# Optimization experiments

Hardware: AMD Instinct MI355X
Metric: run time of the kernel (lower is better)

Reference implementation:

```python
import jax, jax.numpy as jnp
import numpy as np

B, S, H, O, L = 32, 4096, 256, 256, 2


def setup_inputs() -> dict:
    key = jax.random.key(0)
    ks = jax.random.split(key, 12)
    s = 0.05  # weight init scale
    return {
        "input": jax.random.normal(ks[0], (B, S, H), dtype=jnp.float32),
        "hidden_state": jnp.zeros((B, L, H), dtype=jnp.float32),
        # gate weights, stacked over layers: [L, H_out, H_in] (torch Linear convention)
        "Wxz": jax.random.normal(ks[1], (L, H, H), dtype=jnp.float32) * s,
        "Whz": jax.random.normal(ks[2], (L, H, H), dtype=jnp.float32) * s,
        "bz": jax.random.normal(ks[3], (L, H), dtype=jnp.float32) * s,
        "Wxr": jax.random.normal(ks[4], (L, H, H), dtype=jnp.float32) * s,
        "Whr": jax.random.normal(ks[5], (L, H, H), dtype=jnp.float32) * s,
        "br": jax.random.normal(ks[6], (L, H), dtype=jnp.float32) * s,
        "Wxg": jax.random.normal(ks[7], (L, H, H), dtype=jnp.float32) * s,
        "Whg": jax.random.normal(ks[8], (L, H, H), dtype=jnp.float32) * s,
        "bg": jax.random.normal(ks[9], (L, H), dtype=jnp.float32) * s,
        "Why": jax.random.normal(ks[10], (O, H), dtype=jnp.float32) * s,
        "by": jax.random.normal(ks[11], (O,), dtype=jnp.float32) * s,
    }


def _gru_forward(x, h0, Wxz, Whz, bz, Wxr, Whr, br, Wxg, Whg, bg, Why, by):
    # x: [B,S,I], h0: [B,L,H]
    n_layers = Wxz.shape[0]
    xs = jnp.swapaxes(x, 0, 1)          # [S,B,I]
    h_init = jnp.swapaxes(h0, 0, 1)     # [L,B,H]

    def step(h, x_t):                    # h: [L,B,H], x_t: [B,I]
        inp = x_t
        new_h = []
        for l in range(n_layers):
            hl = h[l]
            z = jax.nn.sigmoid(inp @ Wxz[l].T + hl @ Whz[l].T + bz[l])
            r = jax.nn.sigmoid(inp @ Wxr[l].T + hl @ Whr[l].T + br[l])
            g = jnp.tanh(inp @ Wxg[l].T + (hl * r) @ Whg[l].T + bg[l])
            hn = z * hl + (1.0 - z) * g
            new_h.append(hn)
            inp = hn  # dropout p=0 -> identity
        y_t = inp @ Why.T + by           # [B,O]
        return jnp.stack(new_h), y_t

    h_final, ys = jax.lax.scan(step, h_init, xs)
    layer_output = jnp.swapaxes(ys, 0, 1)        # [B,S,O]
    hidden_state = jnp.swapaxes(h_final, 0, 1)   # [B,L,H]
    return layer_output, hidden_state


def reference(input, hidden_state, Wxz, Whz, bz, Wxr, Whr, br, Wxg, Whg, bg, Why, by):
    return _gru_forward(input, hidden_state, Wxz, Whz, bz, Wxr, Whr, br, Wxg, Whg, bg, Why, by)
```

## Files before the change

### kernel.cpp

```cpp
#include <hip/hip_runtime.h>


typedef __attribute__((ext_vector_type(8))) short short8;
typedef __attribute__((ext_vector_type(4))) float f32x4;

#define TC      256
#define NCHUNK  16
#define SSZ     4096
#define LW      (256*256)

#define SIGSC  (-1.44269504089f)
#define TANHSC ( 2.88539008178f)

__device__ __forceinline__ float bf2f(unsigned short u) {
    union { unsigned int i; float f; } v; v.i = ((unsigned int)u) << 16; return v.f;
}
__device__ __forceinline__ unsigned short f2bf(float f) {
    union { float f; unsigned int i; } v; v.f = f;
    v.i += 0x7fff + ((v.i >> 16) & 1);
    return (unsigned short)(v.i >> 16);
}
__device__ __forceinline__ unsigned int pkbf(float lo, float hi) {
    union { float f; unsigned int i; } a, b; a.f = lo; b.f = hi;
    return __builtin_amdgcn_perm(b.i + 0x8000u, a.i + 0x8000u, 0x07060302);
}
__device__ __forceinline__ short8 cvt8s(const float* p, float s) {
    float4 a = *(const float4*)p;
    float4 b = *(const float4*)(p + 4);
    short8 r;
    r[0] = (short)f2bf(a.x * s); r[1] = (short)f2bf(a.y * s);
    r[2] = (short)f2bf(a.z * s); r[3] = (short)f2bf(a.w * s);
    r[4] = (short)f2bf(b.x * s); r[5] = (short)f2bf(b.y * s);
    r[6] = (short)f2bf(b.z * s); r[7] = (short)f2bf(b.w * s);
    return r;
}
__device__ __forceinline__ void wg_barrier() {
    asm volatile("s_waitcnt lgkmcnt(0)" ::: "memory");
    __builtin_amdgcn_s_barrier();
}

__global__ __launch_bounds__(256, 2) void gemm3(
    const float* __restrict__ x,
    const unsigned short* __restrict__ Hc0, const unsigned short* __restrict__ Hc1,
    const float* __restrict__ Wxz, const float* __restrict__ Wxr, const float* __restrict__ Wxg,
    const float* __restrict__ bz,  const float* __restrict__ br,  const float* __restrict__ bg,
    const float* __restrict__ Why, const float* __restrict__ by,
    unsigned short* __restrict__ XS0, unsigned short* __restrict__ XS1,
    float* __restrict__ out, int c)
{
    __shared__ unsigned short Alds[64 * 256];
    __shared__ unsigned short Wlds[64 * 256];

    const int jt = blockIdx.y;
    const void* Aptr; int a_mode, c0abs = 0, o_mode, jtl;
    const float *w0, *w1, *w2, *b0, *b1, *b2; void* Optr;
    if (jt < 12) {
        if (c > 15) return;
        Aptr = x; a_mode = 0; c0abs = c * TC;
        w0 = Wxz; w1 = Wxr; w2 = Wxg; b0 = bz; b1 = br; b2 = bg;
        Optr = XS0; o_mode = 0; jtl = jt;
    } else if (jt < 24) {
        if (c < 1 || c > 16) return;
        Aptr = Hc0; a_mode = 1;
        w0 = Wxz + LW; w1 = Wxr + LW; w2 = Wxg + LW;
        b0 = bz + 256; b1 = br + 256; b2 = bg + 256;
        Optr = XS1; o_mode = 0; jtl = jt - 12;
    } else {
        if (c < 2) return;
        Aptr = Hc1; a_mode = 1; c0abs = (c - 2) * TC;
        w0 = Why; w1 = Why; w2 = Why; b0 = by; b1 = by; b2 = by;
        Optr = out; o_mode = 1; jtl = jt - 24;
    }

    const int tid = threadIdx.x;
    const int mt = blockIdx.x;

    for (int idx = tid; idx < 4096; idx += 256) {
        int row = idx >> 6;
        int kq  = (idx & 63) << 2;
        int sw  = row * 256 + (((((kq >> 3) ^ (row & 7)) << 3)) | (kq & 7));
        if (a_mode == 0) {
            int i = mt * 64 + row; int tc = i >> 5, b = i & 31;
            const float* p = (const float*)Aptr + ((size_t)b * SSZ + (size_t)(c0abs + tc)) * 256 + kq;
            float4 v = *(const float4*)p;
            ushort4 u; u.x = f2bf(v.x); u.y = f2bf(v.y); u.z = f2bf(v.z); u.w = f2bf(v.w);
            *(ushort4*)&Alds[sw] = u;
        } else {
            const unsigned short* p = (const unsigned short*)Aptr + (size_t)(mt * 64 + row) * 256 + kq;
            *(ushort4*)&Alds[sw] = *(const ushort4*)p;
        }
    }
    for (int idx = tid; idx < 4096; idx += 256) {
        int row = idx >> 6;
        int kq  = (idx & 63) << 2;
        int j   = jtl * 64 + row;
        const float* wp = (j < 256) ? w0 : ((j < 512) ? w1 : w2);
        const float* p  = wp + (size_t)(j & 255) * 256 + kq;
        float4 v = *(const float4*)p;
        ushort4 u; u.x = f2bf(v.x); u.y = f2bf(v.y); u.z = f2bf(v.z); u.w = f2bf(v.w);
        int sw = row * 256 + (((((kq >> 3) ^ (row & 7)) << 3)) | (kq & 7));
        *(ushort4*)&Wlds[sw] = u;
    }
    __syncthreads();

    const int lane = tid & 63, wv = tid >> 6;
    const int cl = lane & 15, qr = lane >> 4;
    f32x4 acc[4];
    #pragma unroll
    for (int nt = 0; nt < 4; ++nt) acc[nt] = (f32x4){0.f, 0.f, 0.f, 0.f};

    #pragma unroll
    for (int kt = 0; kt < 8; ++kt) {
        int kb = kt * 4 + qr;
        short8 af = *(const short8*)&Alds[(wv * 16 + cl) * 256 + ((kb ^ (cl & 7)) << 3)];
        #pragma unroll
        for (int nt = 0; nt < 4; ++nt) {
            short8 bf = *(const short8*)&Wlds[(nt * 16 + cl) * 256 + ((kb ^ (cl & 7)) << 3)];
            acc[nt] = __builtin_amdgcn_mfma_f32_16x16x32_bf16(af, bf, acc[nt], 0, 0, 0);
        }
    }

    #pragma unroll
    for (int nt = 0; nt < 4; ++nt) {
        int j = jtl * 64 + nt * 16 + cl;
        const float* bp = (j < 256) ? b0 : ((j < 512) ? b1 : b2);
        float bias = bp[j & 255];
        #pragma unroll
        for (int r = 0; r < 4; ++r) {
            float v = acc[nt][r] + bias;
            int m = mt * 64 + wv * 16 + qr * 4 + r;
            if (o_mode == 0) {
                int t = m >> 5, b = m & 31;
                int wgs = b >> 4, scl = b & 15;
                int gate = j >> 8, cc = j & 255;
                int swv = cc >> 5, snt = (cc >> 4) & 1, sqr = (cc >> 2) & 3, sr = cc & 3;
                int stid = swv * 64 + sqr * 16 + scl;
                size_t off = (((size_t)((t * 2 + wgs) * 3 + gate)) << 12)
                           + (size_t)stid * 8 + (snt * 4 + sr);
                float gs = (gate < 2) ? SIGSC : TANHSC;
                ((unsigned short*)Optr)[off] = f2bf(v * gs);
            } else {
                int tc = m >> 5, b = m & 31;
                ((float*)Optr)[(size_t)b * (SSZ * 256) + (size_t)(c0abs + tc) * 256 + j] = v;
            }
        }
    }
}

__global__ __launch_bounds__(512, 2) void scan_dual(
    const unsigned short* __restrict__ XS0, const unsigned short* __restrict__ XS1,
    unsigned short* __restrict__ Hc0, unsigned short* __restrict__ Hc1,
    float* __restrict__ hstate,
    const float* __restrict__ hidden_in,
    const float* __restrict__ Whz0, const float* __restrict__ Whr0,
    const float* __restrict__ Whg0,
    int c, float* __restrict__ dout_tail)
{
    __shared__ unsigned short hA[4096];
    __shared__ unsigned short A2[4096];
    __shared__ unsigned short Wg[65536];

    const int layer = blockIdx.x >> 1;
    const int wg    = blockIdx.x & 1;
    const int chunk = (layer == 0) ? c : c - 1;
    if (chunk < 0 || chunk > 15) return;

    const unsigned short* XS = (layer == 0) ? XS0 : XS1;
    unsigned short* Hout     = (layer == 0) ? Hc0 : Hc1;
    const float* Whz = Whz0 + (size_t)layer * LW;
    const float* Whr = Whr0 + (size_t)layer * LW;
    const float* Whg = Whg0 + (size_t)layer * LW;
    const int first_chunk = (chunk == 0), last_chunk = (chunk == NCHUNK - 1);

    const int tid  = threadIdx.x;
    const int lane = tid & 63, wv = tid >> 6;
    const int cl   = lane & 15, qr = lane >> 4;
    const int swl  = cl & 7;
    const int b    = wg * 16 + cl;

    for (int idx = tid; idx < 16384; idx += 512) {
        int n  = idx >> 6;
        int kq = (idx & 63) << 2;
        float4 v = *(const float4*)(Whg + (size_t)n * 256 + kq);
        ushort4 u;
        u.x = f2bf(v.x * TANHSC); u.y = f2bf(v.y * TANHSC);
        u.z = f2bf(v.z * TANHSC); u.w = f2bf(v.w * TANHSC);
        int sw = n * 256 + (((((kq >> 3) ^ (n & 7)) << 3)) | (kq & 7));
        *(ushort4*)&Wg[sw] = u;
    }

    short8 wzf[2][8], wrf[2][8];
    #pragma unroll
    for (int nt = 0; nt < 2; ++nt) {
        int n = wv * 32 + nt * 16 + cl;
        #pragma unroll
        for (int kt = 0; kt < 8; ++kt) {
            int k0 = kt * 32 + qr * 8;
            wzf[nt][kt] = cvt8s(Whz + (size_t)n * 256 + k0, SIGSC);
            wrf[nt][kt] = cvt8s(Whr + (size_t)n * 256 + k0, SIGSC);
        }
    }

    int wro[2];
    #pragma unroll
    for (int nt = 0; nt < 2; ++nt) {
        int nb = wv * 32 + nt * 16 + qr * 4;
        wro[nt] = cl * 256 + ((((nb >> 3) ^ swl) << 3) | (nb & 4));
    }

    float hreg[2][4];
    #pragma unroll
    for (int nt = 0; nt < 2; ++nt) {
        int nb = wv * 32 + nt * 16 + qr * 4;
        float4 h4;
        if (first_chunk) h4 = *(const float4*)(hidden_in + (size_t)b * 512 + layer * 256 + nb);
        else             h4 = *(const float4*)(hstate + layer * 8192 + b * 256 + nb);
        hreg[nt][0] = h4.x; hreg[nt][1] = h4.y; hreg[nt][2] = h4.z; hreg[nt][3] = h4.w;
        uint2 p; p.x = pkbf(h4.x, h4.y); p.y = pkbf(h4.z, h4.w);
        *(uint2*)&hA[wro[nt]] = p;
    }

    const unsigned short* xp = XS + (size_t)wg * 12288 + (size_t)tid * 8;
    short8 xz = *(const short8*)(xp);
    short8 xr = *(const short8*)(xp + 4096);
    short8 xg = *(const short8*)(xp + 8192);

    wg_barrier();

    uint2 hpk[2];
    const size_t holane = (size_t)(wg * 16 + cl) * 256 + (size_t)wv * 32 + (size_t)qr * 4;

    #pragma unroll 1
    for (int t = 0; t < TC; ++t) {
        if (t) {
            unsigned short* hp = Hout + (size_t)(t - 1) * 8192 + holane;
            *(uint2*)hp        = hpk[0];
            *(uint2*)(hp + 16) = hpk[1];
        }

        const unsigned short* xq = xp + (size_t)((t + 1 < TC) ? t + 1 : t) * 24576;
        short8 nz = *(const short8*)(xq);
        short8 nr = *(const short8*)(xq + 4096);
        short8 ng = *(const short8*)(xq + 8192);

        f32x4 az[2], ar[2];
        #pragma unroll
        for (int nt = 0; nt < 2; ++nt) {
            #pragma unroll
            for (int r = 0; r < 4; ++r) {
                az[nt][r] = bf2f((unsigned short)xz[nt * 4 + r]);
                ar[nt][r] = bf2f((unsigned short)xr[nt * 4 + r]);
            }
        }
        #pragma unroll
        for (int kt = 0; kt < 8; ++kt) {
            int kb = kt * 4 + qr;
            short8 bf = *(const short8*)&hA[cl * 256 + ((kb ^ swl) << 3)];
            az[0] = __builtin_amdgcn_mfma_f32_16x16x32_bf16(wzf[0][kt], bf, az[0], 0, 0, 0);
            ar[0] = __builtin_amdgcn_mfma_f32_16x16x32_bf16(wrf[0][kt], bf, ar[0], 0, 0, 0);
            az[1] = __builtin_amdgcn_mfma_f32_16x16x32_bf16(wzf[1][kt], bf, az[1], 0, 0, 0);
            ar[1] = __builtin_amdgcn_mfma_f32_16x16x32_bf16(wrf[1][kt], bf, ar[1], 0, 0, 0);
        }

        float zs[2][4];
        #pragma unroll
        for (int nt = 0; nt < 2; ++nt) {
            float a2v[4];
            #pragma unroll
            for (int r = 0; r < 4; ++r) {
                zs[nt][r] = __builtin_amdgcn_rcpf(1.0f + __builtin_amdgcn_exp2f(az[nt][r]));
                float rr  = __builtin_amdgcn_rcpf(1.0f + __builtin_amdgcn_exp2f(ar[nt][r]));
                a2v[r] = rr * hreg[nt][r];
            }
            uint2 p; p.x = pkbf(a2v[0], a2v[1]); p.y = pkbf(a2v[2], a2v[3]);
            *(uint2*)&A2[wro[nt]] = p;
        }
        wg_barrier();

        f32x4 ag[2];
        #pragma unroll
        for (int nt = 0; nt < 2; ++nt) {
            #pragma unroll
            for (int r = 0; r < 4; ++r)
                ag[nt][r] = bf2f((unsigned short)xg[nt * 4 + r]);
        }
        #pragma unroll
        for (int kt = 0; kt < 8; ++kt) {
            int kb = kt * 4 + qr;
            int ko = (kb ^ swl) << 3;
            short8 bf  = *(const short8*)&A2[cl * 256 + ko];
            short8 af0 = *(const short8*)&Wg[(wv * 32 + cl) * 256 + ko];
            short8 af1 = *(const short8*)&Wg[(wv * 32 + 16 + cl) * 256 + ko];
            ag[0] = __builtin_amdgcn_mfma_f32_16x16x32_bf16(af0, bf, ag[0], 0, 0, 0);
            ag[1] = __builtin_amdgcn_mfma_f32_16x16x32_bf16(af1, bf, ag[1], 0, 0, 0);
        }
        #pragma unroll
        for (int nt = 0; nt < 2; ++nt) {
            float hn4[4];
            #pragma unroll
            for (int r = 0; r < 4; ++r) {
                float g = 1.0f - 2.0f * __builtin_amdgcn_rcpf(
                              1.0f + __builtin_amdgcn_exp2f(ag[nt][r]));
                float hn = g + zs[nt][r] * (hreg[nt][r] - g);
                hreg[nt][r] = hn;
                hn4[r] = hn;
            }
            uint2 p; p.x = pkbf(hn4[0], hn4[1]); p.y = pkbf(hn4[2], hn4[3]);
            hpk[nt] = p;
            *(uint2*)&hA[wro[nt]] = p;
        }
        wg_barrier();

        xz = nz; xr = nr; xg = ng;
    }

    {
        unsigned short* hp = Hout + (size_t)(TC - 1) * 8192 + holane;
        *(uint2*)hp        = hpk[0];
        *(uint2*)(hp + 16) = hpk[1];
    }
    #pragma unroll
    for (int nt = 0; nt < 2; ++nt) {
        int nb = wv * 32 + nt * 16 + qr * 4;
        float4 h4; h4.x = hreg[nt][0]; h4.y = hreg[nt][1]; h4.z = hreg[nt][2]; h4.w = hreg[nt][3];
        *(float4*)(hstate + layer * 8192 + b * 256 + nb) = h4;
        if (last_chunk)
            *(float4*)(dout_tail + (size_t)b * 512 + layer * 256 + nb) = h4;
    }
}

extern "C" void kernel_launch(void* const* d_in, const int* in_sizes, int n_in,
                              void* d_out, int out_size, void* d_ws, size_t ws_size,
                              hipStream_t stream) {
    const float* x   = (const float*)d_in[0];
    const float* h0  = (const float*)d_in[1];
    const float* Wxz = (const float*)d_in[2];
    const float* Whz = (const float*)d_in[3];
    const float* bz  = (const float*)d_in[4];
    const float* Wxr = (const float*)d_in[5];
    const float* Whr = (const float*)d_in[6];
    const float* br  = (const float*)d_in[7];
    const float* Wxg = (const float*)d_in[8];
    const float* Whg = (const float*)d_in[9];
    const float* bg  = (const float*)d_in[10];
    const float* Why = (const float*)d_in[11];
    const float* by  = (const float*)d_in[12];
    float* out = (float*)d_out;

    char* ws = (char*)d_ws;
    unsigned short* bufA = (unsigned short*)(ws);
    unsigned short* bufB = (unsigned short*)(ws + 12582912);
    unsigned short* Hc0  = (unsigned short*)(ws + 25165824);
    unsigned short* Hc1  = (unsigned short*)(ws + 29360128);
    float*          hst  = (float*)(ws + 33554432);
    float* dout_tail = out + (size_t)32 * 4096 * 256;

    for (int i = 0; i <= 17; ++i) {
        gemm3<<<dim3(128, 28), 256, 0, stream>>>(x, Hc0, Hc1,
                                                 Wxz, Wxr, Wxg, bz, br, bg,
                                                 Why, by, bufA, bufB, out, i);
        if (i <= 16)
            scan_dual<<<4, 512, 0, stream>>>(bufA, bufB, Hc0, Hc1, hst, h0,
                                             Whz, Whr, Whg, i, dout_tail);
    }
}
```

Measured before the change: 9.550 ms.

## Fuse scan and projection GEMMs into one pipelined kernel with double buffers

```diff
diff --git a/kernel.cpp b/kernel.cpp
--- a/kernel.cpp
+++ b/kernel.cpp
@@ -4,10 +4,12 @@
 typedef __attribute__((ext_vector_type(8))) short short8;
 typedef __attribute__((ext_vector_type(4))) float f32x4;
 
-#define TC      256
-#define NCHUNK  16
+#define TC      128
+#define NCHUNK  32
 #define SSZ     4096
 #define LW      (256*256)
+#define XSPAR   3145728
+#define HPAR    1048576
 
 #define SIGSC  (-1.44269504089f)
 #define TANHSC ( 2.88539008178f)
@@ -39,58 +41,243 @@
     __builtin_amdgcn_s_barrier();
 }
 
-__global__ __launch_bounds__(256, 2) void gemm3(
-    const float* __restrict__ x,
-    const unsigned short* __restrict__ Hc0, const unsigned short* __restrict__ Hc1,
-    const float* __restrict__ Wxz, const float* __restrict__ Wxr, const float* __restrict__ Wxg,
-    const float* __restrict__ bz,  const float* __restrict__ br,  const float* __restrict__ bg,
+struct ScanS {
+    unsigned short hA[4096];
+    unsigned short A2[4096];
+    unsigned short WgL[65536];
+};
+struct GemmS {
+    unsigned short Alds[128 * 256];
+    unsigned short Wlds[64 * 256];
+};
+
+__global__ __launch_bounds__(512, 2) void fused(
+    const float* __restrict__ x, const float* __restrict__ h0,
+    const float* __restrict__ Wxz, const float* __restrict__ Whz, const float* __restrict__ bz,
+    const float* __restrict__ Wxr, const float* __restrict__ Whr, const float* __restrict__ br,
+    const float* __restrict__ Wxg, const float* __restrict__ Whg, const float* __restrict__ bg,
     const float* __restrict__ Why, const float* __restrict__ by,
-    unsigned short* __restrict__ XS0, unsigned short* __restrict__ XS1,
-    float* __restrict__ out, int c)
+    unsigned short* __restrict__ XS0b, unsigned short* __restrict__ XS1b,
+    unsigned short* __restrict__ Hc0b, unsigned short* __restrict__ Hc1b,
+    float* __restrict__ hst, float* __restrict__ out,
+    float* __restrict__ dout_tail, int i)
 {
-    __shared__ unsigned short Alds[64 * 256];
-    __shared__ unsigned short Wlds[64 * 256];
-
-    const int jt = blockIdx.y;
-    const void* Aptr; int a_mode, c0abs = 0, o_mode, jtl;
+    __shared__ union { ScanS s; GemmS g; } sm;
+
+    const int bid = blockIdx.x;
+    const int tid = threadIdx.x;
+
+    if (bid < 4) {
+        const int layer = bid >> 1;
+        const int wg    = bid & 1;
+        const int chunk = (layer == 0) ? i : i - 2;
+        if ((unsigned)chunk > 31u) return;
+
+        const unsigned short* XS = ((layer == 0) ? XS0b : XS1b) + (size_t)(chunk & 1) * XSPAR;
+        unsigned short* Hout     = ((layer == 0) ? Hc0b : Hc1b) + (size_t)(chunk & 1) * HPAR;
+        const float* Whz_l = Whz + (size_t)layer * LW;
+        const float* Whr_l = Whr + (size_t)layer * LW;
+        const float* Whg_l = Whg + (size_t)layer * LW;
+        const int first_chunk = (chunk == 0), last_chunk = (chunk == NCHUNK - 1);
+
+        unsigned short* hA  = sm.s.hA;
+        unsigned short* A2  = sm.s.A2;
+        unsigned short* WgL = sm.s.WgL;
+
+        const int lane = tid & 63, wv = tid >> 6;
+        const int cl   = lane & 15, qr = lane >> 4;
+        const int swl  = cl & 7;
+        const int b    = wg * 16 + cl;
+
+        for (int idx = tid; idx < 8192; idx += 512) {
+            int lane_s = idx & 63, kt = (idx >> 6) & 7, ntv = (idx >> 9) & 1, wvv = idx >> 10;
+            int n  = wvv * 32 + ntv * 16 + (lane_s & 15);
+            int k0 = kt * 32 + (lane_s >> 4) * 8;
+            short8 f = cvt8s(Whg_l + (size_t)n * 256 + k0, TANHSC);
+            *(short8*)&WgL[(size_t)idx * 8] = f;
+        }
+
+        short8 wzf[2][8], wrf[2][8];
+        #pragma unroll
+        for (int nt = 0; nt < 2; ++nt) {
+            int n = wv * 32 + nt * 16 + cl;
+            #pragma unroll
+            for (int kt = 0; kt < 8; ++kt) {
+                int k0 = kt * 32 + qr * 8;
+                wzf[nt][kt] = cvt8s(Whz_l + (size_t)n * 256 + k0, SIGSC);
+                wrf[nt][kt] = cvt8s(Whr_l + (size_t)n * 256 + k0, SIGSC);
+            }
+        }
+
+        int wro[2];
+        #pragma unroll
+        for (int nt = 0; nt < 2; ++nt) {
+            int nb = wv * 32 + nt * 16 + qr * 4;
+            wro[nt] = cl * 256 + ((((nb >> 3) ^ swl) << 3) | (nb & 4));
+        }
+
+        float hreg[2][4];
+        #pragma unroll
+        for (int nt = 0; nt < 2; ++nt) {
+            int nb = wv * 32 + nt * 16 + qr * 4;
+            float4 h4;
+            if (first_chunk) h4 = *(const float4*)(h0 + (size_t)b * 512 + layer * 256 + nb);
+            else             h4 = *(const float4*)(hst + layer * 8192 + b * 256 + nb);
+            hreg[nt][0] = h4.x; hreg[nt][1] = h4.y; hreg[nt][2] = h4.z; hreg[nt][3] = h4.w;
+            uint2 p; p.x = pkbf(h4.x, h4.y); p.y = pkbf(h4.z, h4.w);
+            *(uint2*)&hA[wro[nt]] = p;
+        }
+
+        const unsigned short* xp = XS + (size_t)wg * 12288 + (size_t)tid * 8;
+        short8 xz = *(const short8*)(xp);
+        short8 xr = *(const short8*)(xp + 4096);
+        short8 xg = *(const short8*)(xp + 8192);
+
+        wg_barrier();
+
+        uint2 hpk[2];
+        const size_t holane = (size_t)(wg * 16 + cl) * 256 + (size_t)wv * 32 + (size_t)qr * 4;
+
+        #pragma unroll 1
+        for (int t = 0; t < TC; ++t) {
+            if (t) {
+                unsigned short* hp = Hout + (size_t)(t - 1) * 8192 + holane;
+                *(uint2*)hp        = hpk[0];
+                *(uint2*)(hp + 16) = hpk[1];
+            }
+
+            const unsigned short* xq = xp + (size_t)((t + 1 < TC) ? t + 1 : t) * 24576;
+            short8 nz = *(const short8*)(xq);
+            short8 nr = *(const short8*)(xq + 4096);
+            short8 ng = *(const short8*)(xq + 8192);
+
+            f32x4 az[2], ar[2];
+            #pragma unroll
+            for (int nt = 0; nt < 2; ++nt) {
+                #pragma unroll
+                for (int r = 0; r < 4; ++r) {
+                    az[nt][r] = bf2f((unsigned short)xz[nt * 4 + r]);
+                    ar[nt][r] = bf2f((unsigned short)xr[nt * 4 + r]);
+                }
+            }
+            #pragma unroll
+            for (int kt = 0; kt < 8; ++kt) {
+                int kb = kt * 4 + qr;
+                short8 bf = *(const short8*)&hA[cl * 256 + ((kb ^ swl) << 3)];
+                az[0] = __builtin_amdgcn_mfma_f32_16x16x32_bf16(wzf[0][kt], bf, az[0], 0, 0, 0);
+                ar[0] = __builtin_amdgcn_mfma_f32_16x16x32_bf16(wrf[0][kt], bf, ar[0], 0, 0, 0);
+                az[1] = __builtin_amdgcn_mfma_f32_16x16x32_bf16(wzf[1][kt], bf, az[1], 0, 0, 0);
+                ar[1] = __builtin_amdgcn_mfma_f32_16x16x32_bf16(wrf[1][kt], bf, ar[1], 0, 0, 0);
+            }
+
+            float zs[2][4];
+            #pragma unroll
+            for (int nt = 0; nt < 2; ++nt) {
+                float a2v[4];
+                #pragma unroll
+                for (int r = 0; r < 4; ++r) {
+                    zs[nt][r] = __builtin_amdgcn_rcpf(1.0f + __builtin_amdgcn_exp2f(az[nt][r]));
+                    float rr  = __builtin_amdgcn_rcpf(1.0f + __builtin_amdgcn_exp2f(ar[nt][r]));
+                    a2v[r] = rr * hreg[nt][r];
+                }
+                uint2 p; p.x = pkbf(a2v[0], a2v[1]); p.y = pkbf(a2v[2], a2v[3]);
+                *(uint2*)&A2[wro[nt]] = p;
+            }
+            wg_barrier();
+
+            f32x4 ag[2];
+            #pragma unroll
+            for (int nt = 0; nt < 2; ++nt) {
+                #pragma unroll
+                for (int r = 0; r < 4; ++r)
+                    ag[nt][r] = bf2f((unsigned short)xg[nt * 4 + r]);
+            }
+            #pragma unroll
+            for (int kt = 0; kt < 8; ++kt) {
+                int kb = kt * 4 + qr;
+                int ko = (wv * 16 + kt) * 512 + lane * 8;
+                short8 bf  = *(const short8*)&A2[cl * 256 + ((kb ^ swl) << 3)];
+                short8 af0 = *(const short8*)&WgL[ko];
+                short8 af1 = *(const short8*)&WgL[ko + 4096];
+                ag[0] = __builtin_amdgcn_mfma_f32_16x16x32_bf16(af0, bf, ag[0], 0, 0, 0);
+                ag[1] = __builtin_amdgcn_mfma_f32_16x16x32_bf16(af1, bf, ag[1], 0, 0, 0);
+            }
+            #pragma unroll
+            for (int nt = 0; nt < 2; ++nt) {
+                float hn4[4];
+                #pragma unroll
+                for (int r = 0; r < 4; ++r) {
+                    float g = 1.0f - 2.0f * __builtin_amdgcn_rcpf(
+                                  1.0f + __builtin_amdgcn_exp2f(ag[nt][r]));
+                    float hn = g + zs[nt][r] * (hreg[nt][r] - g);
+                    hreg[nt][r] = hn;
+                    hn4[r] = hn;
+                }
+                uint2 p; p.x = pkbf(hn4[0], hn4[1]); p.y = pkbf(hn4[2], hn4[3]);
+                hpk[nt] = p;
+                *(uint2*)&hA[wro[nt]] = p;
+            }
+            wg_barrier();
+
+            xz = nz; xr = nr; xg = ng;
+        }
+
+        {
+            unsigned short* hp = Hout + (size_t)(TC - 1) * 8192 + holane;
+            *(uint2*)hp        = hpk[0];
+            *(uint2*)(hp + 16) = hpk[1];
+        }
+        #pragma unroll
+        for (int nt = 0; nt < 2; ++nt) {
+            int nb = wv * 32 + nt * 16 + qr * 4;
+            float4 h4; h4.x = hreg[nt][0]; h4.y = hreg[nt][1]; h4.z = hreg[nt][2]; h4.w = hreg[nt][3];
+            *(float4*)(hst + layer * 8192 + b * 256 + nb) = h4;
+            if (last_chunk)
+                *(float4*)(dout_tail + (size_t)b * 512 + layer * 256 + nb) = h4;
+        }
+        return;
+    }
+
+    const int gb = bid - 4;
+    const void* Aptr; int a_mode, c0abs = 0, o_mode, jtl, mtb;
     const float *w0, *w1, *w2, *b0, *b1, *b2; void* Optr;
-    if (jt < 12) {
-        if (c > 15) return;
-        Aptr = x; a_mode = 0; c0abs = c * TC;
+    if (gb < 384) {
+        int c = i + 1; if ((unsigned)c > 31u) return;
+        a_mode = 0; Aptr = x; c0abs = c * TC;
         w0 = Wxz; w1 = Wxr; w2 = Wxg; b0 = bz; b1 = br; b2 = bg;
-        Optr = XS0; o_mode = 0; jtl = jt;
-    } else if (jt < 24) {
-        if (c < 1 || c > 16) return;
-        Aptr = Hc0; a_mode = 1;
+        Optr = XS0b + (size_t)(c & 1) * XSPAR; o_mode = 0; jtl = gb >> 5; mtb = gb & 31;
+    } else if (gb < 768) {
+        int c = i - 1; if ((unsigned)c > 31u) return;
+        a_mode = 1; Aptr = Hc0b + (size_t)(c & 1) * HPAR;
         w0 = Wxz + LW; w1 = Wxr + LW; w2 = Wxg + LW;
         b0 = bz + 256; b1 = br + 256; b2 = bg + 256;
-        Optr = XS1; o_mode = 0; jtl = jt - 12;
+        Optr = XS1b + (size_t)(c & 1) * XSPAR; o_mode = 0; jtl = (gb - 384) >> 5; mtb = (gb - 384) & 31;
     } else {
-        if (c < 2) return;
-        Aptr = Hc1; a_mode = 1; c0abs = (c - 2) * TC;
+        int c = i - 3; if ((unsigned)c > 31u) return;
+        a_mode = 1; Aptr = Hc1b + (size_t)(c & 1) * HPAR; c0abs = c * TC;
         w0 = Why; w1 = Why; w2 = Why; b0 = by; b1 = by; b2 = by;
-        Optr = out; o_mode = 1; jtl = jt - 24;
-    }
-
-    const int tid = threadIdx.x;
-    const int mt = blockIdx.x;
-
-    for (int idx = tid; idx < 4096; idx += 256) {
+        Optr = out; o_mode = 1; jtl = (gb - 768) >> 5; mtb = (gb - 768) & 31;
+    }
+
+    unsigned short* Alds = sm.g.Alds;
+    unsigned short* Wlds = sm.g.Wlds;
+
+    for (int idx = tid; idx < 8192; idx += 512) {
         int row = idx >> 6;
         int kq  = (idx & 63) << 2;
         int sw  = row * 256 + (((((kq >> 3) ^ (row & 7)) << 3)) | (kq & 7));
         if (a_mode == 0) {
-            int i = mt * 64 + row; int tc = i >> 5, b = i & 31;
-            const float* p = (const float*)Aptr + ((size_t)b * SSZ + (size_t)(c0abs + tc)) * 256 + kq;
+            int i0 = mtb * 128 + row; int tc = i0 >> 5, bb = i0 & 31;
+            const float* p = (const float*)Aptr + ((size_t)bb * SSZ + (size_t)(c0abs + tc)) * 256 + kq;
             float4 v = *(const float4*)p;
             ushort4 u; u.x = f2bf(v.x); u.y = f2bf(v.y); u.z = f2bf(v.z); u.w = f2bf(v.w);
             *(ushort4*)&Alds[sw] = u;
         } else {
-            const unsigned short* p = (const unsigned short*)Aptr + (size_t)(mt * 64 + row) * 256 + kq;
+            const unsigned short* p = (const unsigned short*)Aptr + (size_t)(mtb * 128 + row) * 256 + kq;
             *(ushort4*)&Alds[sw] = *(const ushort4*)p;
         }
     }
-    for (int idx = tid; idx < 4096; idx += 256) {
+    for (int idx = tid; idx < 4096; idx += 512) {
         int row = idx >> 6;
         int kq  = (idx & 63) << 2;
         int j   = jtl * 64 + row;
@@ -105,6 +292,7 @@
 
     const int lane = tid & 63, wv = tid >> 6;
     const int cl = lane & 15, qr = lane >> 4;
+    const int sub = wv >> 2, wq = wv & 3;
     f32x4 acc[4];
     #pragma unroll
     for (int nt = 0; nt < 4; ++nt) acc[nt] = (f32x4){0.f, 0.f, 0.f, 0.f};
@@ -112,7 +300,7 @@
     #pragma unroll
     for (int kt = 0; kt < 8; ++kt) {
         int kb = kt * 4 + qr;
-        short8 af = *(const short8*)&Alds[(wv * 16 + cl) * 256 + ((kb ^ (cl & 7)) << 3)];
+        short8 af = *(const short8*)&Alds[(sub * 64 + wq * 16 + cl) * 256 + ((kb ^ (cl & 7)) << 3)];
         #pragma unroll
         for (int nt = 0; nt < 4; ++nt) {
             short8 bf = *(const short8*)&Wlds[(nt * 16 + cl) * 256 + ((kb ^ (cl & 7)) << 3)];
@@ -128,10 +316,10 @@
         #pragma unroll
         for (int r = 0; r < 4; ++r) {
             float v = acc[nt][r] + bias;
-            int m = mt * 64 + wv * 16 + qr * 4 + r;
+            int m = mtb * 128 + sub * 64 + wq * 16 + qr * 4 + r;
             if (o_mode == 0) {
-                int t = m >> 5, b = m & 31;
-                int wgs = b >> 4, scl = b & 15;
+                int t = m >> 5, bb = m & 31;
+                int wgs = bb >> 4, scl = bb & 15;
                 int gate = j >> 8, cc = j & 255;
                 int swv = cc >> 5, snt = (cc >> 4) & 1, sqr = (cc >> 2) & 3, sr = cc & 3;
                 int stid = swv * 64 + sqr * 16 + scl;
@@ -140,192 +328,10 @@
                 float gs = (gate < 2) ? SIGSC : TANHSC;
                 ((unsigned short*)Optr)[off] = f2bf(v * gs);
             } else {
-                int tc = m >> 5, b = m & 31;
-                ((float*)Optr)[(size_t)b * (SSZ * 256) + (size_t)(c0abs + tc) * 256 + j] = v;
-            }
-        }
-    }
-}
-
-__global__ __launch_bounds__(512, 2) void scan_dual(
-    const unsigned short* __restrict__ XS0, const unsigned short* __restrict__ XS1,
-    unsigned short* __restrict__ Hc0, unsigned short* __restrict__ Hc1,
-    float* __restrict__ hstate,
-    const float* __restrict__ hidden_in,
-    const float* __restrict__ Whz0, const float* __restrict__ Whr0,
-    const float* __restrict__ Whg0,
-    int c, float* __restrict__ dout_tail)
-{
-    __shared__ unsigned short hA[4096];
-    __shared__ unsigned short A2[4096];
-    __shared__ unsigned short Wg[65536];
-
-    const int layer = blockIdx.x >> 1;
-    const int wg    = blockIdx.x & 1;
-    const int chunk = (layer == 0) ? c : c - 1;
-    if (chunk < 0 || chunk > 15) return;
-
-    const unsigned short* XS = (layer == 0) ? XS0 : XS1;
-    unsigned short* Hout     = (layer == 0) ? Hc0 : Hc1;
-    const float* Whz = Whz0 + (size_t)layer * LW;
-    const float* Whr = Whr0 + (size_t)layer * LW;
-    const float* Whg = Whg0 + (size_t)layer * LW;
-    const int first_chunk = (chunk == 0), last_chunk = (chunk == NCHUNK - 1);
-
-    const int tid  = threadIdx.x;
-    const int lane = tid & 63, wv = tid >> 6;
-    const int cl   = lane & 15, qr = lane >> 4;
-    const int swl  = cl & 7;
-    const int b    = wg * 16 + cl;
-
-    for (int idx = tid; idx < 16384; idx += 512) {
-        int n  = idx >> 6;
-        int kq = (idx & 63) << 2;
-        float4 v = *(const float4*)(Whg + (size_t)n * 256 + kq);
-        ushort4 u;
-        u.x = f2bf(v.x * TANHSC); u.y = f2bf(v.y * TANHSC);
-        u.z = f2bf(v.z * TANHSC); u.w = f2bf(v.w * TANHSC);
-        int sw = n * 256 + (((((kq >> 3) ^ (n & 7)) << 3)) | (kq & 7));
-        *(ushort4*)&Wg[sw] = u;
-    }
-
-    short8 wzf[2][8], wrf[2][8];
-    #pragma unroll
-    for (int nt = 0; nt < 2; ++nt) {
-        int n = wv * 32 + nt * 16 + cl;
-        #pragma unroll
-        for (int kt = 0; kt < 8; ++kt) {
-            int k0 = kt * 32 + qr * 8;
-            wzf[nt][kt] = cvt8s(Whz + (size_t)n * 256 + k0, SIGSC);
-            wrf[nt][kt] = cvt8s(Whr + (size_t)n * 256 + k0, SIGSC);
-        }
-    }
-
-    int wro[2];
-    #pragma unroll
-    for (int nt = 0; nt < 2; ++nt) {
-        int nb = wv * 32 + nt * 16 + qr * 4;
-        wro[nt] = cl * 256 + ((((nb >> 3) ^ swl) << 3) | (nb & 4));
-    }
-
-    float hreg[2][4];
-    #pragma unroll
-    for (int nt = 0; nt < 2; ++nt) {
-        int nb = wv * 32 + nt * 16 + qr * 4;
-        float4 h4;
-        if (first_chunk) h4 = *(const float4*)(hidden_in + (size_t)b * 512 + layer * 256 + nb);
-        else             h4 = *(const float4*)(hstate + layer * 8192 + b * 256 + nb);
-        hreg[nt][0] = h4.x; hreg[nt][1] = h4.y; hreg[nt][2] = h4.z; hreg[nt][3] = h4.w;
-        uint2 p; p.x = pkbf(h4.x, h4.y); p.y = pkbf(h4.z, h4.w);
-        *(uint2*)&hA[wro[nt]] = p;
-    }
-
-    const unsigned short* xp = XS + (size_t)wg * 12288 + (size_t)tid * 8;
-    short8 xz = *(const short8*)(xp);
-    short8 xr = *(const short8*)(xp + 4096);
-    short8 xg = *(const short8*)(xp + 8192);
-
-    wg_barrier();
-
-    uint2 hpk[2];
-    const size_t holane = (size_t)(wg * 16 + cl) * 256 + (size_t)wv * 32 + (size_t)qr * 4;
-
-    #pragma unroll 1
-    for (int t = 0; t < TC; ++t) {
-        if (t) {
-            unsigned short* hp = Hout + (size_t)(t - 1) * 8192 + holane;
-            *(uint2*)hp        = hpk[0];
-            *(uint2*)(hp + 16) = hpk[1];
-        }
-
-        const unsigned short* xq = xp + (size_t)((t + 1 < TC) ? t + 1 : t) * 24576;
-        short8 nz = *(const short8*)(xq);
-        short8 nr = *(const short8*)(xq + 4096);
-        short8 ng = *(const short8*)(xq + 8192);
-
-        f32x4 az[2], ar[2];
-        #pragma unroll
-        for (int nt = 0; nt < 2; ++nt) {
-            #pragma unroll
-            for (int r = 0; r < 4; ++r) {
-                az[nt][r] = bf2f((unsigned short)xz[nt * 4 + r]);
-                ar[nt][r] = bf2f((unsigned short)xr[nt * 4 + r]);
-            }
-        }
-        #pragma unroll
-        for (int kt = 0; kt < 8; ++kt) {
-            int kb = kt * 4 + qr;
-            short8 bf = *(const short8*)&hA[cl * 256 + ((kb ^ swl) << 3)];
-            az[0] = __builtin_amdgcn_mfma_f32_16x16x32_bf16(wzf[0][kt], bf, az[0], 0, 0, 0);
-            ar[0] = __builtin_amdgcn_mfma_f32_16x16x32_bf16(wrf[0][kt], bf, ar[0], 0, 0, 0);
-            az[1] = __builtin_amdgcn_mfma_f32_16x16x32_bf16(wzf[1][kt], bf, az[1], 0, 0, 0);
-            ar[1] = __builtin_amdgcn_mfma_f32_16x16x32_bf16(wrf[1][kt], bf, ar[1], 0, 0, 0);
-        }
-
-        float zs[2][4];
-        #pragma unroll
-        for (int nt = 0; nt < 2; ++nt) {
-            float a2v[4];
-            #pragma unroll
-            for (int r = 0; r < 4; ++r) {
-                zs[nt][r] = __builtin_amdgcn_rcpf(1.0f + __builtin_amdgcn_exp2f(az[nt][r]));
-                float rr  = __builtin_amdgcn_rcpf(1.0f + __builtin_amdgcn_exp2f(ar[nt][r]));
-                a2v[r] = rr * hreg[nt][r];
-            }
-            uint2 p; p.x = pkbf(a2v[0], a2v[1]); p.y = pkbf(a2v[2], a2v[3]);
-            *(uint2*)&A2[wro[nt]] = p;
-        }
-        wg_barrier();
-
-        f32x4 ag[2];
-        #pragma unroll
-        for (int nt = 0; nt < 2; ++nt) {
-            #pragma unroll
-            for (int r = 0; r < 4; ++r)
-                ag[nt][r] = bf2f((unsigned short)xg[nt * 4 + r]);
-        }
-        #pragma unroll
-        for (int kt = 0; kt < 8; ++kt) {
-            int kb = kt * 4 + qr;
-            int ko = (kb ^ swl) << 3;
-            short8 bf  = *(const short8*)&A2[cl * 256 + ko];
-            short8 af0 = *(const short8*)&Wg[(wv * 32 + cl) * 256 + ko];
-            short8 af1 = *(const short8*)&Wg[(wv * 32 + 16 + cl) * 256 + ko];
-            ag[0] = __builtin_amdgcn_mfma_f32_16x16x32_bf16(af0, bf, ag[0], 0, 0, 0);
-            ag[1] = __builtin_amdgcn_mfma_f32_16x16x32_bf16(af1, bf, ag[1], 0, 0, 0);
-        }
-        #pragma unroll
-        for (int nt = 0; nt < 2; ++nt) {
-            float hn4[4];
-            #pragma unroll
-            for (int r = 0; r < 4; ++r) {
-                float g = 1.0f - 2.0f * __builtin_amdgcn_rcpf(
-                              1.0f + __builtin_amdgcn_exp2f(ag[nt][r]));
-                float hn = g + zs[nt][r] * (hreg[nt][r] - g);
-                hreg[nt][r] = hn;
-                hn4[r] = hn;
-            }
-            uint2 p; p.x = pkbf(hn4[0], hn4[1]); p.y = pkbf(hn4[2], hn4[3]);
-            hpk[nt] = p;
-            *(uint2*)&hA[wro[nt]] = p;
-        }
-        wg_barrier();
-
-        xz = nz; xr = nr; xg = ng;
-    }
-
-    {
-        unsigned short* hp = Hout + (size_t)(TC - 1) * 8192 + holane;
-        *(uint2*)hp        = hpk[0];
-        *(uint2*)(hp + 16) = hpk[1];
-    }
-    #pragma unroll
-    for (int nt = 0; nt < 2; ++nt) {
-        int nb = wv * 32 + nt * 16 + qr * 4;
-        float4 h4; h4.x = hreg[nt][0]; h4.y = hreg[nt][1]; h4.z = hreg[nt][2]; h4.w = hreg[nt][3];
-        *(float4*)(hstate + layer * 8192 + b * 256 + nb) = h4;
-        if (last_chunk)
-            *(float4*)(dout_tail + (size_t)b * 512 + layer * 256 + nb) = h4;
+                int tc = m >> 5, bb = m & 31;
+                ((float*)Optr)[(size_t)bb * (SSZ * 256) + (size_t)(c0abs + tc) * 256 + j] = v;
+            }
+        }
     }
 }
 
@@ -355,12 +361,11 @@
     float*          hst  = (float*)(ws + 33554432);
     float* dout_tail = out + (size_t)32 * 4096 * 256;
 
-    for (int i = 0; i <= 17; ++i) {
-        gemm3<<<dim3(128, 28), 256, 0, stream>>>(x, Hc0, Hc1,
-                                                 Wxz, Wxr, Wxg, bz, br, bg,
-                                                 Why, by, bufA, bufB, out, i);
-        if (i <= 16)
-            scan_dual<<<4, 512, 0, stream>>>(bufA, bufB, Hc0, Hc1, hst, h0,
-                                             Whz, Whr, Whg, i, dout_tail);
-    }
-}
+    for (int i = -1; i <= 34; ++i) {
+        fused<<<dim3(900), 512, 0, stream>>>(x, h0,
+                                             Wxz, Whz, bz, Wxr, Whr, br,
+                                             Wxg, Whg, bg, Why, by,
+                                             bufA, bufB, Hc0, Hc1,
+                                             hst, out, dout_tail, i);
+    }
+}
```

Result: faster. 7.978 ms (-16.5%).
